# Optimization experiments

Hardware: AMD Instinct MI355X
Metric: run time of the kernel (lower is better)

## Reference

```python
import jax, jax.numpy as jnp
import numpy as np

NPERSEG = 512
STEP = 256
NSEG = 9            # frames for L=2048 with boundary='zeros', padded=True
NFREQ = 257
NUM_FILTER = 2
PI = 3.1415926      # same constant as source

_win = 0.5 * (1.0 - jnp.cos(2.0 * jnp.pi * jnp.arange(NPERSEG, dtype=jnp.float32) / NPERSEG))  # periodic hann (scipy get_window('hann'))
_win_sum = 256.0    # sum of periodic hann, exact


def _stft(x):
    # x: (B, D, L) real -> scipy.signal.stft(..., nperseg=512, noverlap=256) => (B, D, 257, 9)
    xp = jnp.pad(x, ((0, 0), (0, 0), (STEP, STEP)))  # boundary='zeros'
    idx = jnp.arange(NSEG)[:, None] * STEP + jnp.arange(NPERSEG)[None, :]
    frames = xp[..., idx] * _win                     # (B,D,9,512)
    Z = jnp.fft.rfft(frames, axis=-1) / _win_sum     # scaling='spectrum'
    return jnp.swapaxes(Z, -1, -2)                   # (B,D,257,9)


def _istft(Z):
    # Z: (B,D,257,9) complex -> (B,D,2048) real (scipy.signal.istft inverse)
    xs = jnp.fft.irfft(jnp.swapaxes(Z, -1, -2) * _win_sum, n=NPERSEG, axis=-1) * _win  # (B,D,9,512)
    total = NPERSEG + (NSEG - 1) * STEP  # 2560
    idx = (jnp.arange(NSEG)[:, None] * STEP + jnp.arange(NPERSEG)[None, :]).reshape(-1)
    B, D = Z.shape[0], Z.shape[1]
    x = jnp.zeros((B, D, total), xs.dtype).at[..., idx].add(xs.reshape(B, D, -1))
    norm = jnp.zeros((total,), jnp.float32).at[idx].add(jnp.tile(_win ** 2, NSEG))
    x = x / jnp.where(norm > 1e-10, norm, 1.0)
    return x[..., STEP:total - STEP]  # trim boundary padding -> length 2048


def _cplx(p):
    return p[..., 0] + 1j * p[..., 1]  # torch.view_as_complex


def _filter(x, length, bank):
    # x: (B,S,D) complex; bank: (K,S,D,2). power = x*x/length (complex square, as in source)
    power = x * x / length
    k = jnp.arange(NUM_FILTER, dtype=jnp.float32)
    coef = jnp.cos((2.0 * (k + 1.0) - 1.0) * PI / 2.0 * NUM_FILTER)  # matches source precedence
    return jnp.sum(power[None] * _cplx(bank)[:, None] * coef[:, None, None, None], axis=0)


def _ln(x, g, b):
    m = jnp.mean(x, -1, keepdims=True)
    v = jnp.mean((x - m) ** 2, -1, keepdims=True)
    return (x - m) * jax.lax.rsqrt(v + 1e-5) * g + b


def _addnorm(x, g1, b1, w1, bb1, w2, bb2, g2, b2):
    x = _ln(x, g1, b1)
    h = jax.nn.gelu(x @ w1.T + bb1, approximate=False)  # torch GELU (exact)
    return _ln(h @ w2.T + bb2 + x, g2, b2)


def setup_inputs() -> dict:
    key = jax.random.key(0)
    ks = jax.random.split(key, 12)
    B, D = 8, 768
    d = {}
    d['ecg'] = jax.random.normal(ks[0], (B, 2048, D), jnp.float32)
    d['image'] = jax.random.normal(ks[1], (B, 196, D), jnp.float32)
    d['ecg_filter_bank'] = jax.random.normal(ks[2], (2, 2313, D, 2), jnp.float32)
    d['cxr_filter_bank'] = jax.random.normal(ks[3], (2, 99, D, 2), jnp.float32)
    d['gate_sel'] = jax.random.normal(ks[4], (99, D, 2), jnp.float32)
    d['gate_w'] = jax.random.normal(ks[5], (D, D), jnp.float32) * 0.02
    d['gate_b'] = jnp.zeros((D,), jnp.float32)
    for i, p in enumerate(['e', 'c']):
        d[p + '_ln1_g'] = jnp.ones((D,), jnp.float32)
        d[p + '_ln1_b'] = jnp.zeros((D,), jnp.float32)
        d[p + '_w1'] = jax.random.normal(ks[6 + 2 * i], (D, D), jnp.float32) * 0.02
        d[p + '_b1'] = jnp.zeros((D,), jnp.float32)
        d[p + '_w2'] = jax.random.normal(ks[7 + 2 * i], (D, D), jnp.float32) * 0.02
        d[p + '_b2'] = jnp.zeros((D,), jnp.float32)
        d[p + '_ln2_g'] = jnp.ones((D,), jnp.float32)
        d[p + '_ln2_b'] = jnp.zeros((D,), jnp.float32)
    return d


def reference(ecg, image, ecg_filter_bank, cxr_filter_bank, gate_sel, gate_w, gate_b,
              e_ln1_g, e_ln1_b, e_w1, e_b1, e_w2, e_b2, e_ln2_g, e_ln2_b,
              c_ln1_g, c_ln1_b, c_w1, c_b1, c_w2, c_b2, c_ln2_g, c_ln2_b):
    B, S, D = ecg.shape
    N = image.shape[1]
    # STFT path (source detaches to CPU -> stop_gradient)
    Z = _stft(jnp.swapaxes(jax.lax.stop_gradient(ecg), 1, 2))       # (B,D,257,9)
    _ecg = jnp.transpose(Z, (0, 2, 3, 1)).reshape(B, NFREQ * NSEG, D)
    _img = jnp.fft.rfft(image, axis=1, norm='ortho')                # (B,99,D)
    _ecg = _filter(_ecg, NFREQ * NSEG, ecg_filter_bank)
    _img = _filter(_img, N // 2 + 1, cxr_filter_bank)
    # Cxr2EcgGate: complex selection, avgpool over spatial (real part), 1x1 conv
    gate = jnp.mean((_img * _cplx(gate_sel)).real, axis=1) @ gate_w.T + gate_b  # (B,D)
    ecg_g = _ecg * gate[:, None, :]
    # NOTE: source overwrites gated image with irfft of filtered _image (ecg_gate output unused)
    img_t = jnp.fft.irfft(_img, n=N, axis=1, norm='ortho')          # (B,N,D)
    Zg = jnp.transpose(ecg_g.reshape(B, NFREQ, NSEG, D), (0, 3, 1, 2))
    ecg_t = jnp.swapaxes(_istft(jax.lax.stop_gradient(Zg)), 1, 2)   # (B,2048,D); source detaches before istft
    text = _addnorm(ecg_t + ecg, e_ln1_g, e_ln1_b, e_w1, e_b1, e_w2, e_b2, e_ln2_g, e_ln2_b)
    img = _addnorm(img_t + image, c_ln1_g, c_ln1_b, c_w1, c_b1, c_w2, c_b2, c_ln2_g, c_ln2_b)
    return (text, img)
```

## Files before the change

kernel.cpp:

```cpp
#include <hip/hip_runtime.h>
#include <math.h>

namespace {

constexpr int B_ = 8;
constexpr int S_ = 2048;
constexpr int D_ = 768;
constexpr int N_ = 196;
constexpr int NF_ = 99;
constexpr int NFREQ_ = 257;
constexpr int NSEG_ = 9;
constexpr int NBINS_ = NFREQ_ * NSEG_;
constexpr int NW_ = D_ * D_;
constexpr float TWOPI_ = 6.28318530717958647692f;

using bf16x8 = __attribute__((ext_vector_type(8))) short;
using f32x4  = __attribute__((ext_vector_type(4))) float;

__device__ __forceinline__ int rev9(int x) { return (int)(__brev((unsigned)x) >> 23); }
__device__ __forceinline__ int padz(int i) { return i + (i >> 4); }

__device__ __forceinline__ unsigned short f2bf(float x) {
  unsigned u = __float_as_uint(x);
  u = (u + 0x7FFFu + ((u >> 16) & 1u)) >> 16;
  return (unsigned short)u;
}
__device__ __forceinline__ float bf2f(unsigned short h) {
  return __uint_as_float(((unsigned)h) << 16);
}

__device__ __forceinline__ float gelu_f(float v) {
  const float x = fabsf(v) * 0.70710678118654752440f;
  const float t = 1.0f / fmaf(0.3275911f, x, 1.0f);
  float p = fmaf(fmaf(fmaf(fmaf(1.061405429f, t, -1.453152027f), t, 1.421413741f),
                      t, -0.284496736f), t, 0.254829592f);
  const float e = __expf(-x * x);
  const float er = 1.0f - p * t * e;
  return 0.5f * v * (1.0f + ((v < 0.f) ? -er : er));
}

__device__ __forceinline__ void gload16(const void* g, void* l) {
  __builtin_amdgcn_global_load_lds((const __attribute__((address_space(1))) void*)g,
                                   (__attribute__((address_space(3))) void*)l, 16, 0, 0);
}

__device__ __forceinline__ float2 cmulf(float2 a, float2 b) {
  return make_float2(a.x * b.x - a.y * b.y, a.x * b.y + a.y * b.x);
}
__device__ __forceinline__ float2 cadd(float2 a, float2 b) {
  return make_float2(a.x + b.x, a.y + b.y);
}
__device__ __forceinline__ float2 csub(float2 a, float2 b) {
  return make_float2(a.x - b.x, a.y - b.y);
}

__global__ __launch_bounds__(256) void k_transpose_g(const float* __restrict__ src,
                                                     float* __restrict__ dst,
                                                     int R, int C) {
  __shared__ float tile[32][33];
  const int b = blockIdx.z;
  const int c0 = blockIdx.x * 32;
  const int r0 = blockIdx.y * 32;
  const int tx = threadIdx.x & 31, ty = threadIdx.x >> 5;
  for (int i = ty; i < 32; i += 8)
    tile[i][tx] = src[((size_t)b * R + r0 + i) * C + c0 + tx];
  __syncthreads();
  for (int i = ty; i < 32; i += 8)
    dst[((size_t)b * C + c0 + i) * R + r0 + tx] = tile[tx][i];
}

constexpr int PREP_W = (NW_ + 255) / 256;
constexpr int PREP_WALL = 4 * PREP_W;
constexpr int PREP_FC = (NBINS_ * D_ + 255) / 256;
__global__ __launch_bounds__(256) void k_prep(
    const float* __restrict__ w0, const float* __restrict__ w1,
    const float* __restrict__ w2, const float* __restrict__ w3,
    unsigned short* __restrict__ wbf, const float2* __restrict__ e2,
    float2* __restrict__ FcT, float2* __restrict__ twg) {
  const int bid = blockIdx.x;
  if (bid < PREP_WALL) {
    const int m = bid / PREP_W;
    const int i = (bid - m * PREP_W) * 256 + threadIdx.x;
    if (i >= NW_) return;
    const float* src = (m == 0) ? w0 : (m == 1) ? w1 : (m == 2) ? w2 : w3;
    wbf[(size_t)m * NW_ + i] = f2bf(src[i]);
  } else if (bid < PREP_WALL + PREP_FC) {
    const int o = (bid - PREP_WALL) * 256 + threadIdx.x;
    if (o >= NBINS_ * D_) return;
    const int d = o / NBINS_;
    const int r = o - d * NBINS_;
    const int f = r / NFREQ_;
    const int k = r - f * NFREQ_;
    const int s = k * 9 + f;
    const float2 a = e2[(size_t)s * D_ + d];
    const float2 b = e2[(size_t)(NBINS_ + s) * D_ + d];
    FcT[o] = make_float2(-(a.x + b.x), -(a.y + b.y));
  } else {
    const int i = (bid - PREP_WALL - PREP_FC) * 256 + threadIdx.x;
    if (i >= 511) return;
    const int v = i + 1;
    const int h = 1 << (31 - __clz(v));
    const int j = v - h;
    float sn, cs;
    sincosf((float)j * ((TWOPI_ * 0.5f) / (float)h), &sn, &cs);
    twg[i] = make_float2(cs, sn);
  }
}

__global__ __launch_bounds__(256) void k_img_dft_f(
    const float* __restrict__ image, const float2* __restrict__ bank2,
    const float2* __restrict__ gsel2, float2* __restrict__ imgF,
    float* __restrict__ part) {
  const int fg = blockIdx.x;
  const int f0 = fg * 9;
  const int d = blockIdx.y * 256 + threadIdx.x;
  const int b = blockIdx.z;
  __shared__ float2 tws[9 * N_];
  for (int idx = threadIdx.x; idx < 9 * N_; idx += 256) {
    const int fi = idx / N_;
    const int t = idx - fi * N_;
    const int r = ((f0 + fi) * t) % N_;
    float sn, cs;
    sincosf(TWOPI_ * (float)r / (float)N_, &sn, &cs);
    tws[idx] = make_float2(cs, sn);
  }
  __syncthreads();
  float re[9] = {}, im[9] = {};
  const float* ip = image + (size_t)b * N_ * D_ + d;
  for (int t = 0; t < N_; ++t) {
    const float v = ip[(size_t)t * D_];
#pragma unroll
    for (int fi = 0; fi < 9; ++fi) {
      const float2 w = tws[fi * N_ + t];
      re[fi] = fmaf(v, w.x, re[fi]);
      im[fi] = fmaf(-v, w.y, im[fi]);
    }
  }
  const float sc = 1.0f / (196.0f * 99.0f);
  float gp = 0.f;
#pragma unroll
  for (int fi = 0; fi < 9; ++fi) {
    const int f = f0 + fi;
    const float pr = (re[fi] * re[fi] - im[fi] * im[fi]) * sc;
    const float pi2 = (2.f * re[fi] * im[fi]) * sc;
    const size_t fd = (size_t)f * D_ + d;
    const float2 c0 = bank2[fd];
    const float2 c1 = bank2[(size_t)NF_ * D_ + fd];
    const float fcr = -(c0.x + c1.x), fci = -(c0.y + c1.y);
    const float zr = pr * fcr - pi2 * fci;
    const float zi = pr * fci + pi2 * fcr;
    imgF[(size_t)(b * NF_ + f) * D_ + d] = make_float2(zr, zi);
    const float2 gw = gsel2[fd];
    gp += zr * gw.x - zi * gw.y;
  }
  part[((size_t)b * 11 + fg) * D_ + d] = gp;
}

__global__ __launch_bounds__(256) void k_gate_mm2(const float* __restrict__ part,
                                                  const float* __restrict__ W,
                                                  const float* __restrict__ bias,
                                                  float* __restrict__ gate) {
  __shared__ float row[8][D_];
  __shared__ float red[16][16][8];
  const int tid = threadIdx.x;
  const int d0 = blockIdx.x * 16;
  for (int i = tid; i < 8 * D_; i += 256) {
    const int b = i / D_, e = i - b * D_;
    float s = 0.f;
    for (int p = 0; p < 11; ++p) s += part[((size_t)b * 11 + p) * D_ + e];
    row[b][e] = s * (1.0f / 99.0f);
  }
  __syncthreads();
  const int dl = tid >> 4;
  const int ec = tid & 15;
  const float* w = W + (size_t)(d0 + dl) * D_ + ec * 48;
  float acc[8] = {};
  for (int e = 0; e < 48; e += 4) {
    const float4 wv = *reinterpret_cast<const float4*>(w + e);
    const int eg = ec * 48 + e;
#pragma unroll
    for (int b = 0; b < 8; ++b) {
      acc[b] = fmaf(row[b][eg], wv.x, acc[b]);
      acc[b] = fmaf(row[b][eg + 1], wv.y, acc[b]);
      acc[b] = fmaf(row[b][eg + 2], wv.z, acc[b]);
      acc[b] = fmaf(row[b][eg + 3], wv.w, acc[b]);
    }
  }
#pragma unroll
  for (int b = 0; b < 8; ++b) red[dl][ec][b] = acc[b];
  __syncthreads();
  if (tid < 128) {
    const int dl2 = tid >> 3, b = tid & 7;
    float s = bias[d0 + dl2];
    for (int c = 0; c < 16; ++c) s += red[dl2][c][b];
    gate[b * D_ + d0 + dl2] = s;
  }
}

__global__ __launch_bounds__(256) void k_img_idft(
    const float2* __restrict__ imgF, const float* __restrict__ image,
    float* __restrict__ xi) {
  const int t0 = blockIdx.x * 14;
  const int d = blockIdx.y * 256 + threadIdx.x;
  const int b = blockIdx.z;
  __shared__ float2 tws[14 * NF_];
  for (int idx = threadIdx.x; idx < 14 * NF_; idx += 256) {
    const int ti = idx / NF_;
    const int f = idx - ti * NF_;
    const int r = ((t0 + ti) * f) % N_;
    float sn, cs;
    sincosf(TWOPI_ * (float)r / (float)N_, &sn, &cs);
    tws[idx] = make_float2(cs, sn);
  }
  __syncthreads();
  const float2* zp = imgF + (size_t)b * NF_ * D_ + d;
  const float2 z0 = zp[0];
  const float2 zny = zp[(size_t)(NF_ - 1) * D_];
  float acc[14];
#pragma unroll
  for (int ti = 0; ti < 14; ++ti)
    acc[ti] = z0.x + (((t0 + ti) & 1) ? -zny.x : zny.x);
  for (int f = 1; f < NF_ - 1; ++f) {
    const float2 z = zp[(size_t)f * D_];
#pragma unroll
    for (int ti = 0; ti < 14; ++ti) {
      const float2 w = tws[ti * NF_ + f];
      acc[ti] += 2.f * (z.x * w.x - z.y * w.y);
    }
  }
#pragma unroll
  for (int ti = 0; ti < 14; ++ti) {
    const size_t idx = (size_t)(b * N_ + t0 + ti) * D_ + d;
    xi[idx] = acc[ti] * (1.0f / 14.0f) + image[idx];
  }
}

__global__ __launch_bounds__(256) void k_layernorm_f2b(const float* __restrict__ x,
                                                       const float* __restrict__ g,
                                                       const float* __restrict__ b,
                                                       unsigned short* __restrict__ out) {
  const int row = blockIdx.x;
  const int tid = threadIdx.x;
  const float* xr = x + (size_t)row * D_;
  const float v0 = xr[tid], v1 = xr[tid + 256], v2 = xr[tid + 512];
  float s = v0 + v1 + v2;
  float q = v0 * v0 + v1 * v1 + v2 * v2;
  __shared__ float red[8];
  for (int off = 32; off > 0; off >>= 1) {
    s += __shfl_down(s, off);
    q += __shfl_down(q, off);
  }
  if ((tid & 63) == 0) { red[tid >> 6] = s; red[4 + (tid >> 6)] = q; }
  __syncthreads();
  s = red[0] + red[1] + red[2] + red[3];
  q = red[4] + red[5] + red[6] + red[7];
  const float mean = s * (1.0f / 768.0f);
  const float var = q * (1.0f / 768.0f) - mean * mean;
  const float inv = rsqrtf(var + 1e-5f);
  unsigned short* orow = out + (size_t)row * D_;
  orow[tid]       = f2bf((v0 - mean) * inv * g[tid]       + b[tid]);
  orow[tid + 256] = f2bf((v1 - mean) * inv * g[tid + 256] + b[tid + 256]);
  orow[tid + 512] = f2bf((v2 - mean) * inv * g[tid + 512] + b[tid + 512]);
}

template <int H, int DIR, bool TRIV>
__device__ __forceinline__ void pass8(float2* z, int l,
                                      float2 wa, float2 wb, float2 wc) {
  asm volatile("s_waitcnt lgkmcnt(0)" ::: "memory");
  const float sg = (DIR < 0) ? -1.f : 1.f;
  const int base = (H == 1) ? (l << 3)
                 : (H == 8) ? (((l >> 3) << 6) | (l & 7))
                            : l;
  const float2 x0 = z[padz(base)],         x1 = z[padz(base + H)];
  const float2 x2 = z[padz(base + 2 * H)], x3 = z[padz(base + 3 * H)];
  const float2 x4 = z[padz(base + 4 * H)], x5 = z[padz(base + 5 * H)];
  const float2 x6 = z[padz(base + 6 * H)], x7 = z[padz(base + 7 * H)];
  const float2 WA = make_float2(wa.x, sg * wa.y);
  const float2 WB = make_float2(wb.x, sg * wb.y);
  const float2 WC = make_float2(wc.x, sg * wc.y);
  const float2 WBp = make_float2(-sg * WB.y, sg * WB.x);
  float2 t, u;
  t = TRIV ? x1 : cmulf(x1, WA); const float2 A0 = cadd(x0, t), A1 = csub(x0, t);
  t = TRIV ? x3 : cmulf(x3, WA); const float2 A2 = cadd(x2, t), A3 = csub(x2, t);
  t = TRIV ? x5 : cmulf(x5, WA); const float2 A4 = cadd(x4, t), A5 = csub(x4, t);
  t = TRIV ? x7 : cmulf(x7, WA); const float2 A6 = cadd(x6, t), A7 = csub(x6, t);
  t = TRIV ? A2 : cmulf(A2, WB);
  u = TRIV ? make_float2(-sg * A3.y, sg * A3.x) : cmulf(A3, WBp);
  const float2 B0 = cadd(A0, t), B2 = csub(A0, t);
  const float2 B1 = cadd(A1, u), B3 = csub(A1, u);
  t = TRIV ? A6 : cmulf(A6, WB);
  u = TRIV ? make_float2(-sg * A7.y, sg * A7.x) : cmulf(A7, WBp);
  const float2 B4 = cadd(A4, t), B6 = csub(A4, t);
  const float2 B5 = cadd(A5, u), B7 = csub(A5, u);
  const float r_ = 0.70710678118654752440f;
  const float2 F1 = TRIV ? make_float2(r_, sg * r_)
                         : cmulf(WC, make_float2(r_, sg * r_));
  const float2 F2 = TRIV ? make_float2(0.f, sg)
                         : make_float2(-sg * WC.y, sg * WC.x);
  const float2 F3 = TRIV ? make_float2(-r_, sg * r_)
                         : cmulf(WC, make_float2(-r_, sg * r_));
  t = TRIV ? B4 : cmulf(B4, WC);
  z[padz(base)]         = cadd(B0, t);
  z[padz(base + 4 * H)] = csub(B0, t);
  t = cmulf(B5, F1);
  z[padz(base + H)]     = cadd(B1, t);
  z[padz(base + 5 * H)] = csub(B1, t);
  t = cmulf(B6, F2);
  z[padz(base + 2 * H)] = cadd(B2, t);
  z[padz(base + 6 * H)] = csub(B2, t);
  t = cmulf(B7, F3);
  z[padz(base + 3 * H)] = cadd(B3, t);
  z[padz(base + 7 * H)] = csub(B3, t);
}

template <int FA, int FB>
__device__ __forceinline__ void filt_pack(const float2* z, int k, float g,
                                          float2 cA, float2 cB,
                                          float2& Ck, float2& Cm) {
  const int q = (512 - k) & 511;
  const float2 Zk = z[padz(k)], Zq = z[padz(q)];
  const float sc = 0.5f / 256.f;
  const float ar = (Zk.x + Zq.x) * sc, ai = (Zk.y - Zq.y) * sc;
  float yar, yai, ybr = 0.f, ybi = 0.f;
  {
    const float pr = (ar * ar - ai * ai) * (1.f / 2313.f);
    const float pi = (2.f * ar * ai) * (1.f / 2313.f);
    yar = (pr * cA.x - pi * cA.y) * g;
    yai = (pr * cA.y + pi * cA.x) * g;
  }
  if (FB >= 0) {
    const float br = (Zk.y + Zq.y) * sc, bi = (Zq.x - Zk.x) * sc;
    const float pr = (br * br - bi * bi) * (1.f / 2313.f);
    const float pi = (2.f * br * bi) * (1.f / 2313.f);
    ybr = (pr * cB.x - pi * cB.y) * g;
    ybi = (pr * cB.y + pi * cB.x) * g;
  }
  if (k == 0 || k == 256) {
    Ck = make_float2(yar, ybr);
    Cm = Ck;
  } else {
    Ck = make_float2(yar - ybi, yai + ybr);
    Cm = make_float2(yar + ybi, ybr - yai);
  }
}

template <int FA0, int FB0, int FA1, int FB1, bool DUAL>
__device__ __forceinline__ void ecg_super(int tid, float g, const float2* __restrict__ fc,
                                          const float (&s)[8], const float2 (&ptw)[6],
                                          float2 t8, float2* zA, float2* zB, float* accr) {
  const float c0 = t8.x;
  const float wlo = 0.5f - 0.5f * c0;
  const float whi = 0.5f + 0.5f * c0;
  const float2 cA0 = fc[FA0 * 257 + tid];
  float2 cB0 = make_float2(0.f, 0.f), cA1 = cB0, cB1 = cB0;
  if (FB0 >= 0) cB0 = fc[FB0 * 257 + tid];
  if (DUAL) { cA1 = fc[FA1 * 257 + tid]; cB1 = fc[FB1 * 257 + tid]; }
  float2 nA0 = make_float2(0.f, 0.f), nB0 = nA0, nA1 = nA0, nB1 = nA0;
  if (tid == 0) {
    nA0 = fc[FA0 * 257 + 256];
    if (FB0 >= 0) nB0 = fc[FB0 * 257 + 256];
    if (DUAL) { nA1 = fc[FA1 * 257 + 256]; nB1 = fc[FB1 * 257 + 256]; }
  }
  __syncthreads();
  {
    constexpr int iAlo = (FA0 > 0) ? FA0 - 1 : 0;
    constexpr int iAhi = (FA0 < 8) ? FA0 : 0;
    constexpr int iBlo = (FB0 > 0) ? FB0 - 1 : 0;
    constexpr int iBhi = (FB0 >= 0 && FB0 < 8) ? FB0 : 0;
    const int rlo = padz(rev9(tid)), rhi = padz(rev9(tid + 256));
    const float aLo = (FA0 == 0) ? 0.f : s[iAlo] * wlo;
    const float aHi = (FA0 == 8) ? 0.f : s[iAhi] * whi;
    const float bLo = (FB0 <= 0) ? 0.f : s[iBlo] * wlo;
    const float bHi = (FB0 < 0 || FB0 == 8) ? 0.f : s[iBhi] * whi;
    zA[rlo] = make_float2(aLo, bLo);
    zA[rhi] = make_float2(aHi, bHi);
    if (DUAL) {
      constexpr int jAlo = (FA1 > 0) ? FA1 - 1 : 0;
      constexpr int jAhi = (FA1 < 8) ? FA1 : 0;
      constexpr int jBlo = (FB1 > 0) ? FB1 - 1 : 0;
      constexpr int jBhi = (FB1 < 8) ? FB1 : 0;
      const float eLo = (FA1 == 0) ? 0.f : s[jAlo] * wlo;
      const float eHi = (FA1 == 8) ? 0.f : s[jAhi] * whi;
      const float fLo = (FB1 == 0) ? 0.f : s[jBlo] * wlo;
      const float fHi = (FB1 == 8) ? 0.f : s[jBhi] * whi;
      zB[rlo] = make_float2(eLo, fLo);
      zB[rhi] = make_float2(eHi, fHi);
    }
  }
  __syncthreads();
  if (tid < 64 || (DUAL && tid >= 128 && tid < 192)) {
    float2* zz = (tid < 64) ? zA : zB;
    const int l = tid & 63;
    pass8<1, -1, true>(zz, l, ptw[0], ptw[1], ptw[2]);
    pass8<8, -1, false>(zz, l, ptw[0], ptw[1], ptw[2]);
    pass8<64, -1, false>(zz, l, ptw[3], ptw[4], ptw[5]);
  }
  __syncthreads();
  float2 CAk, CAm, CBk, CBm;
  filt_pack<FA0, FB0>(zA, tid, g, cA0, cB0, CAk, CAm);
  float2 CAn, CBn, dum;
  if (tid == 0) filt_pack<FA0, FB0>(zA, 256, g, nA0, nB0, CAn, dum);
  if (DUAL) {
    filt_pack<FA1, FB1>(zB, tid, g, cA1, cB1, CBk, CBm);
    if (tid == 0) filt_pack<FA1, FB1>(zB, 256, g, nA1, nB1, CBn, dum);
  }
  __syncthreads();
  {
    const int rk = padz(rev9(tid));
    zA[rk] = CAk;
    if (DUAL) zB[rk] = CBk;
    if (tid == 0) {
      zA[padz(1)] = CAn;
      if (DUAL) zB[padz(1)] = CBn;
    } else {
      const int rm = padz(rev9(512 - tid));
      zA[rm] = CAm;
      if (DUAL) zB[rm] = CBm;
    }
  }
  __syncthreads();
  if (tid < 64 || (DUAL && tid >= 128 && tid < 192)) {
    float2* zz = (tid < 64) ? zA : zB;
    const int l = tid & 63;
    pass8<1, 1, true>(zz, l, ptw[0], ptw[1], ptw[2]);
    pass8<8, 1, false>(zz, l, ptw[0], ptw[1], ptw[2]);
    pass8<64, 1, false>(zz, l, ptw[3], ptw[4], ptw[5]);
  }
  __syncthreads();
  {
    const float2 vLo = zA[padz(tid)], vHi = zA[padz(tid + 256)];
    accr[FA0] += 0.5f * wlo * vLo.x;
    accr[FA0 + 1] += 0.5f * whi * vHi.x;
    if (FB0 >= 0) {
      accr[FB0] += 0.5f * wlo * vLo.y;
      accr[FB0 + 1] += 0.5f * whi * vHi.y;
    }
    if (DUAL) {
      const float2 uLo = zB[padz(tid)], uHi = zB[padz(tid + 256)];
      accr[FA1] += 0.5f * wlo * uLo.x;
      accr[FA1 + 1] += 0.5f * whi * uHi.x;
      accr[FB1] += 0.5f * wlo * uLo.y;
      accr[FB1 + 1] += 0.5f * whi * uHi.y;
    }
  }
}

__global__ __launch_bounds__(256) void k_ecg_fft(
    const float* __restrict__ ecgT, const float2* __restrict__ FcT,
    const float* __restrict__ gate, const float2* __restrict__ twg,
    unsigned short* __restrict__ xtT) {
  const int bd = blockIdx.x;
  const int d = bd % D_;
  const int tid = threadIdx.x;

  __shared__ float2 zA[544], zB[544];

  float s[8];
  const float* src = ecgT + (size_t)bd * S_;
#pragma unroll
  for (int k = 0; k < 8; ++k) s[k] = src[k * 256 + tid];

  const int l6 = tid & 63;
  float2 ptw[6];
  ptw[0] = twg[7 + (l6 & 7)];
  ptw[1] = twg[15 + (l6 & 7)];
  ptw[2] = twg[31 + (l6 & 7)];
  ptw[3] = twg[63 + l6];
  ptw[4] = twg[127 + l6];
  ptw[5] = twg[255 + l6];
  const float2 t8 = twg[255 + tid];

  const float g = gate[bd];
  const float2* fc = FcT + (size_t)d * NBINS_;
  float accr[10];
#pragma unroll
  for (int i = 0; i < 10; ++i) accr[i] = 0.f;

  ecg_super<0, 8, 1, 2, true>(tid, g, fc, s, ptw, t8, zA, zB, accr);
  ecg_super<3, 4, 5, 6, true>(tid, g, fc, s, ptw, t8, zA, zB, accr);
  ecg_super<7, -1, 0, 0, false>(tid, g, fc, s, ptw, t8, zA, zB, accr);

  const float c0 = t8.x;
  const float rinv = 1.0f / (0.5f + 0.5f * c0 * c0);
  unsigned short* dst = xtT + (size_t)bd * S_;
#pragma unroll
  for (int i2 = 0; i2 < 8; ++i2)
    dst[i2 * 256 + tid] = f2bf(accr[i2 + 1] * rinv + s[i2]);
}

__global__ __launch_bounds__(256) void k_colstats_bf(const unsigned short* __restrict__ xtT,
                                                     float2* __restrict__ stats) {
  const int b = blockIdx.y;
  const int t0 = blockIdx.x * 128;
  const int tx = threadIdx.x & 63;
  const int ty = threadIdx.x >> 6;
  float s0 = 0.f, q0 = 0.f, s1 = 0.f, q1 = 0.f;
  const unsigned int* base = (const unsigned int*)(xtT + (size_t)b * D_ * S_);
  for (int dd = ty; dd < D_; dd += 4) {
    const unsigned int u = base[(size_t)dd * (S_ / 2) + (t0 >> 1) + tx];
    const float v0 = bf2f((unsigned short)(u & 0xffffu));
    const float v1 = bf2f((unsigned short)(u >> 16));
    s0 += v0; q0 = fmaf(v0, v0, q0);
    s1 += v1; q1 = fmaf(v1, v1, q1);
  }
  __shared__ float sh[4][64][4];
  sh[ty][tx][0] = s0; sh[ty][tx][1] = q0; sh[ty][tx][2] = s1; sh[ty][tx][3] = q1;
  __syncthreads();
  if (ty == 0) {
    s0 = sh[0][tx][0] + sh[1][tx][0] + sh[2][tx][0] + sh[3][tx][0];
    q0 = sh[0][tx][1] + sh[1][tx][1] + sh[2][tx][1] + sh[3][tx][1];
    s1 = sh[0][tx][2] + sh[1][tx][2] + sh[2][tx][2] + sh[3][tx][2];
    q1 = sh[0][tx][3] + sh[1][tx][3] + sh[2][tx][3] + sh[3][tx][3];
    stats[(size_t)b * S_ + t0 + 2 * tx]     = make_float2(s0, q0);
    stats[(size_t)b * S_ + t0 + 2 * tx + 1] = make_float2(s1, q1);
  }
}

__global__ __launch_bounds__(256) void k_transpose_ln(
    const unsigned short* __restrict__ xtT, const float2* __restrict__ stats,
    const float* __restrict__ g, const float* __restrict__ bia,
    unsigned short* __restrict__ xhat) {
  __shared__ float tile[32][33];
  const int b = blockIdx.z;
  const int t0 = blockIdx.x * 32;
  const int d0 = blockIdx.y * 32;
  const int tx = threadIdx.x & 31, ty = threadIdx.x >> 5;
  for (int i = ty; i < 32; i += 8)
    tile[i][tx] = bf2f(xtT[((size_t)b * D_ + d0 + i) * S_ + t0 + tx]);
  __syncthreads();
  const float gv = g[d0 + tx], bv = bia[d0 + tx];
  for (int i = ty; i < 32; i += 8) {
    const float2 st = stats[(size_t)b * S_ + t0 + i];
    const float mean = st.x * (1.0f / 768.0f);
    const float var = st.y * (1.0f / 768.0f) - mean * mean;
    const float inv = rsqrtf(var + 1e-5f);
    xhat[((size_t)b * S_ + t0 + i) * D_ + d0 + tx] =
        f2bf((tile[tx][i] - mean) * inv * gv + bv);
  }
}

__global__ __launch_bounds__(256) void k_layernorm_bf(const unsigned short* __restrict__ x,
                                                      const float* __restrict__ g,
                                                      const float* __restrict__ b,
                                                      float* __restrict__ out) {
  const int row = blockIdx.x;
  const int tid = threadIdx.x;
  const unsigned short* xr = x + (size_t)row * D_;
  const float v0 = bf2f(xr[tid]), v1 = bf2f(xr[tid + 256]), v2 = bf2f(xr[tid + 512]);
  float s = v0 + v1 + v2;
  float q = v0 * v0 + v1 * v1 + v2 * v2;
  __shared__ float red[8];
  for (int off = 32; off > 0; off >>= 1) {
    s += __shfl_down(s, off);
    q += __shfl_down(q, off);
  }
  if ((tid & 63) == 0) { red[tid >> 6] = s; red[4 + (tid >> 6)] = q; }
  __syncthreads();
  s = red[0] + red[1] + red[2] + red[3];
  q = red[4] + red[5] + red[6] + red[7];
  const float mean = s * (1.0f / 768.0f);
  const float var = q * (1.0f / 768.0f) - mean * mean;
  const float inv = rsqrtf(var + 1e-5f);
  float* orow = out + (size_t)row * D_;
  orow[tid]       = (v0 - mean) * inv * g[tid]       + b[tid];
  orow[tid + 256] = (v1 - mean) * inv * g[tid + 256] + b[tid + 256];
  orow[tid + 512] = (v2 - mean) * inv * g[tid + 512] + b[tid + 512];
}

template <int MODE, bool SWZ>
__global__ __launch_bounds__(256) void k_gemm_mfma(
    const unsigned short* __restrict__ Abf, const unsigned short* __restrict__ Wbf,
    const float* __restrict__ bias, const unsigned short* __restrict__ resid,
    unsigned short* __restrict__ outb, int M) {
  __shared__ unsigned short Asm[2][128 * 64];
  __shared__ unsigned short Bsm[2][128 * 64];
  const int tid = threadIdx.x;
  const int lane = tid & 63, wid = tid >> 6;
  const int wr = wid >> 1, wc = wid & 1;
  int bx = blockIdx.x, by = blockIdx.y;
  if (SWZ) {
    const int nwg = gridDim.x * gridDim.y;
    const int bid = by * gridDim.x + bx;
    const int nbid = (bid % 8) * (nwg >> 3) + (bid >> 3);
    bx = nbid % gridDim.x;
    by = nbid / gridDim.x;
  }
  const int n0 = bx * 128, m0 = by * 128;

  auto STAGE = [&](int buf, int kt) {
    const int k0 = kt * 64;
#pragma unroll
    for (int i = 0; i < 4; ++i) {
      const int c = tid + 256 * i;
      const int row = c >> 3, sl = c & 7;
      const int gsl = sl ^ (row & 7);
      gload16(Abf + (size_t)(m0 + row) * 768 + k0 + gsl * 8, &Asm[buf][c * 8]);
      gload16(Wbf + (size_t)(n0 + row) * 768 + k0 + gsl * 8, &Bsm[buf][c * 8]);
    }
  };

  f32x4 acc[4][4] = {};
  STAGE(0, 0);
  for (int kt = 0; kt < 12; ++kt) {
    const int cur = kt & 1;
    if (kt < 11) {
      STAGE(cur ^ 1, kt + 1);
      asm volatile("s_waitcnt vmcnt(8)" ::: "memory");
    } else {
      asm volatile("s_waitcnt vmcnt(0)" ::: "memory");
    }
    __builtin_amdgcn_sched_barrier(0);
    __builtin_amdgcn_s_barrier();
#pragma unroll
    for (int ks = 0; ks < 2; ++ks) {
      bf16x8 af[4], bfv[4];
#pragma unroll
      for (int mi = 0; mi < 4; ++mi) {
        const int row = wr * 64 + mi * 16 + (lane & 15);
        const int sl = (ks * 4 + (lane >> 4)) ^ (row & 7);
        af[mi] = *(const bf16x8*)((const char*)Asm[cur] + row * 128 + sl * 16);
      }
#pragma unroll
      for (int ni = 0; ni < 4; ++ni) {
        const int row = wc * 64 + ni * 16 + (lane & 15);
        const int sl = (ks * 4 + (lane >> 4)) ^ (row & 7);
        bfv[ni] = *(const bf16x8*)((const char*)Bsm[cur] + row * 128 + sl * 16);
      }
#pragma unroll
      for (int mi = 0; mi < 4; ++mi)
#pragma unroll
        for (int ni = 0; ni < 4; ++ni)
          acc[mi][ni] = __builtin_amdgcn_mfma_f32_16x16x32_bf16(af[mi], bfv[ni],
                                                                acc[mi][ni], 0, 0, 0);
    }
    __builtin_amdgcn_sched_barrier(0);
    __builtin_amdgcn_s_barrier();
  }
#pragma unroll
  for (int mi = 0; mi < 4; ++mi) {
#pragma unroll
    for (int ni = 0; ni < 4; ++ni) {
      const int col = n0 + wc * 64 + ni * 16 + (lane & 15);
#pragma unroll
      for (int e = 0; e < 4; ++e) {
        const int row = m0 + wr * 64 + mi * 16 + (lane >> 4) * 4 + e;
        if (row >= M) continue;
        float v = acc[mi][ni][e] + bias[col];
        if (MODE == 0) {
          v = gelu_f(v);
        } else {
          v += bf2f(resid[(size_t)row * 768 + col]);
        }
        outb[(size_t)row * 768 + col] = f2bf(v);
      }
    }
  }
}

}

extern "C" void kernel_launch(void* const* d_in, const int* in_sizes, int n_in,
                              void* d_out, int out_size, void* d_ws, size_t ws_size,
                              hipStream_t stream) {
  (void)in_sizes; (void)n_in; (void)out_size; (void)ws_size;
  const float* ecg     = (const float*)d_in[0];
  const float* image   = (const float*)d_in[1];
  const float* ebank   = (const float*)d_in[2];
  const float* cbank   = (const float*)d_in[3];
  const float* gsel    = (const float*)d_in[4];
  const float* gw      = (const float*)d_in[5];
  const float* gb      = (const float*)d_in[6];
  const float* e_ln1_g = (const float*)d_in[7];
  const float* e_ln1_b = (const float*)d_in[8];
  const float* e_w1    = (const float*)d_in[9];
  const float* e_b1    = (const float*)d_in[10];
  const float* e_w2    = (const float*)d_in[11];
  const float* e_b2    = (const float*)d_in[12];
  const float* e_ln2_g = (const float*)d_in[13];
  const float* e_ln2_b = (const float*)d_in[14];
  const float* c_ln1_g = (const float*)d_in[15];
  const float* c_ln1_b = (const float*)d_in[16];
  const float* c_w1    = (const float*)d_in[17];
  const float* c_b1    = (const float*)d_in[18];
  const float* c_w2    = (const float*)d_in[19];
  const float* c_b2    = (const float*)d_in[20];
  const float* c_ln2_g = (const float*)d_in[21];
  const float* c_ln2_b = (const float*)d_in[22];

  float* out = (float*)d_out;
  float* ws = (float*)d_ws;

  constexpr size_t TXT = (size_t)8 * 2048 * 768;
  constexpr size_t IMG = (size_t)8 * 196 * 768;

  float* A  = ws;
  float* Bb = A + TXT;
  unsigned short* wbf = (unsigned short*)(Bb + TXT);
  unsigned short* ew1b = wbf;
  unsigned short* ew2b = wbf + NW_;
  unsigned short* cw1b = wbf + 2 * NW_;
  unsigned short* cw2b = wbf + 3 * NW_;
  float* gatev = (float*)(wbf + 4 * (size_t)NW_);
  float2* stats = (float2*)(gatev + 8 * 768);
  float* gpart = (float*)(stats + 8 * 2048);
  float2* twg = (float2*)(gpart + 8 * 11 * 768);

  float2* FcT = (float2*)out;

  float* xi = A;
  unsigned short* xh_i = (unsigned short*)(A + IMG);
  unsigned short* h_i  = xh_i + IMG;
  unsigned short* y_ib = h_i + IMG;

  unsigned short* xhat = (unsigned short*)A;
  unsigned short* y_tb = (unsigned short*)A + TXT;
  unsigned short* xtT  = (unsigned short*)Bb;
  unsigned short* h_t  = (unsigned short*)Bb;

  k_prep<<<PREP_WALL + PREP_FC + 2, 256, 0, stream>>>(
      e_w1, e_w2, c_w1, c_w2, wbf, (const float2*)ebank, FcT, twg);

  k_img_dft_f<<<dim3(11, 3, 8), 256, 0, stream>>>(image, (const float2*)cbank,
                                                  (const float2*)gsel,
                                                  (float2*)(A + 2 * IMG), gpart);
  k_gate_mm2<<<48, 256, 0, stream>>>(gpart, gw, gb, gatev);
  k_img_idft<<<dim3(14, 3, 8), 256, 0, stream>>>((const float2*)(A + 2 * IMG), image, xi);
  k_layernorm_f2b<<<1568, 256, 0, stream>>>(xi, c_ln1_g, c_ln1_b, xh_i);
  k_gemm_mfma<0, false><<<dim3(6, 13), 256, 0, stream>>>(xh_i, cw1b, c_b1, nullptr, h_i, 1568);
  k_gemm_mfma<1, false><<<dim3(6, 13), 256, 0, stream>>>(h_i, cw2b, c_b2, xh_i, y_ib, 1568);
  k_layernorm_bf<<<1568, 256, 0, stream>>>(y_ib, c_ln2_g, c_ln2_b, out + TXT);

  k_transpose_g<<<dim3(24, 64, 8), 256, 0, stream>>>(ecg, A, 2048, 768);
  k_ecg_fft<<<8 * 768, 256, 0, stream>>>(A, FcT, gatev, twg, xtT);
  k_colstats_bf<<<dim3(16, 8), 256, 0, stream>>>(xtT, stats);
  k_transpose_ln<<<dim3(64, 24, 8), 256, 0, stream>>>(xtT, stats, e_ln1_g, e_ln1_b, xhat);

  k_gemm_mfma<0, true><<<dim3(6, 128), 256, 0, stream>>>(xhat, ew1b, e_b1, nullptr, h_t, 16384);
  k_gemm_mfma<1, true><<<dim3(6, 128), 256, 0, stream>>>(h_t, ew2b, e_b2, xhat, y_tb, 16384);
  k_layernorm_bf<<<16384, 256, 0, stream>>>(y_tb, e_ln2_g, e_ln2_b, out);
}
```

Baseline: 474.6 us.

## Batch four FFT buffers per pass and merge image/ECG GEMM and layernorm launches

The ECG STFT kernel now processes four frame-pair buffers per super-step using all four wavefronts, so two super-steps replace three and fewer block barriers are needed. The image-branch GEMMs and final layernorm are merged into the ECG-branch launches through dual-problem kernels that pick operands by block index. This removes small under-filled launches, and the GEMM gets an XCD swizzle that handles block counts not divisible by 8. To avoid overlap, the image buffers are moved into the upper half of the second workspace. The cost is more shared memory per FFT block, which may lower occupancy.

```diff
diff --git a/kernel.cpp b/kernel.cpp
--- a/kernel.cpp
+++ b/kernel.cpp
@@ -314,6 +314,21 @@
 }
 
 template <int FA, int FB>
+__device__ __forceinline__ void scatter_buf(float2* z, const float (&s)[8],
+                                            float wlo, float whi, int rlo, int rhi) {
+  constexpr int iAlo = (FA > 0) ? FA - 1 : 0;
+  constexpr int iAhi = (FA < 8) ? FA : 0;
+  constexpr int iBlo = (FB > 0) ? FB - 1 : 0;
+  constexpr int iBhi = (FB >= 0 && FB < 8) ? FB : 0;
+  const float aLo = (FA == 0) ? 0.f : s[iAlo] * wlo;
+  const float aHi = (FA == 8) ? 0.f : s[iAhi] * whi;
+  const float bLo = (FB <= 0) ? 0.f : s[iBlo] * wlo;
+  const float bHi = (FB < 0 || FB == 8) ? 0.f : s[iBhi] * whi;
+  z[rlo] = make_float2(aLo, bLo);
+  z[rhi] = make_float2(aHi, bHi);
+}
+
+template <int FA, int FB>
 __device__ __forceinline__ void filt_pack(const float2* z, int k, float g,
                                           float2 cA, float2 cB,
                                           float2& Ck, float2& Cm) {
@@ -344,84 +359,84 @@
   }
 }
 
-template <int FA0, int FB0, int FA1, int FB1, bool DUAL>
-__device__ __forceinline__ void ecg_super(int tid, float g, const float2* __restrict__ fc,
-                                          const float (&s)[8], const float2 (&ptw)[6],
-                                          float2 t8, float2* zA, float2* zB, float* accr) {
+template <int FA0, int FB0, int FA1, int FB1, int FA2, int FB2, int FA3, int FB3,
+          int NBUF>
+__device__ __forceinline__ void ecg_super4(int tid, float g,
+                                           const float2* __restrict__ fc,
+                                           const float (&s)[8], const float2 (&ptw)[6],
+                                           float2 t8, float2* zA, float2* zB,
+                                           float2* zC, float2* zD, float* accr) {
   const float c0 = t8.x;
   const float wlo = 0.5f - 0.5f * c0;
   const float whi = 0.5f + 0.5f * c0;
-  const float2 cA0 = fc[FA0 * 257 + tid];
+  float2 cA0 = fc[FA0 * 257 + tid];
   float2 cB0 = make_float2(0.f, 0.f), cA1 = cB0, cB1 = cB0;
+  float2 cA2 = cB0, cB2 = cB0, cA3 = cB0, cB3 = cB0;
   if (FB0 >= 0) cB0 = fc[FB0 * 257 + tid];
-  if (DUAL) { cA1 = fc[FA1 * 257 + tid]; cB1 = fc[FB1 * 257 + tid]; }
-  float2 nA0 = make_float2(0.f, 0.f), nB0 = nA0, nA1 = nA0, nB1 = nA0;
-  if (tid == 0) {
-    nA0 = fc[FA0 * 257 + 256];
-    if (FB0 >= 0) nB0 = fc[FB0 * 257 + 256];
-    if (DUAL) { nA1 = fc[FA1 * 257 + 256]; nB1 = fc[FB1 * 257 + 256]; }
-  }
-  __syncthreads();
-  {
-    constexpr int iAlo = (FA0 > 0) ? FA0 - 1 : 0;
-    constexpr int iAhi = (FA0 < 8) ? FA0 : 0;
-    constexpr int iBlo = (FB0 > 0) ? FB0 - 1 : 0;
-    constexpr int iBhi = (FB0 >= 0 && FB0 < 8) ? FB0 : 0;
-    const int rlo = padz(rev9(tid)), rhi = padz(rev9(tid + 256));
-    const float aLo = (FA0 == 0) ? 0.f : s[iAlo] * wlo;
-    const float aHi = (FA0 == 8) ? 0.f : s[iAhi] * whi;
-    const float bLo = (FB0 <= 0) ? 0.f : s[iBlo] * wlo;
-    const float bHi = (FB0 < 0 || FB0 == 8) ? 0.f : s[iBhi] * whi;
-    zA[rlo] = make_float2(aLo, bLo);
-    zA[rhi] = make_float2(aHi, bHi);
-    if (DUAL) {
-      constexpr int jAlo = (FA1 > 0) ? FA1 - 1 : 0;
-      constexpr int jAhi = (FA1 < 8) ? FA1 : 0;
-      constexpr int jBlo = (FB1 > 0) ? FB1 - 1 : 0;
-      constexpr int jBhi = (FB1 < 8) ? FB1 : 0;
-      const float eLo = (FA1 == 0) ? 0.f : s[jAlo] * wlo;
-      const float eHi = (FA1 == 8) ? 0.f : s[jAhi] * whi;
-      const float fLo = (FB1 == 0) ? 0.f : s[jBlo] * wlo;
-      const float fHi = (FB1 == 8) ? 0.f : s[jBhi] * whi;
-      zB[rlo] = make_float2(eLo, fLo);
-      zB[rhi] = make_float2(eHi, fHi);
-    }
-  }
-  __syncthreads();
-  if (tid < 64 || (DUAL && tid >= 128 && tid < 192)) {
-    float2* zz = (tid < 64) ? zA : zB;
-    const int l = tid & 63;
+  if (NBUF > 1) { cA1 = fc[FA1 * 257 + tid]; cB1 = fc[FB1 * 257 + tid]; }
+  if (NBUF > 2) { cA2 = fc[FA2 * 257 + tid]; cB2 = fc[FB2 * 257 + tid]; }
+  if (NBUF > 3) { cA3 = fc[FA3 * 257 + tid]; cB3 = fc[FB3 * 257 + tid]; }
+  __syncthreads();
+  const int rlo = padz(rev9(tid)), rhi = padz(rev9(tid + 256));
+  scatter_buf<FA0, FB0>(zA, s, wlo, whi, rlo, rhi);
+  if (NBUF > 1) scatter_buf<FA1, FB1>(zB, s, wlo, whi, rlo, rhi);
+  if (NBUF > 2) scatter_buf<FA2, FB2>(zC, s, wlo, whi, rlo, rhi);
+  if (NBUF > 3) scatter_buf<FA3, FB3>(zD, s, wlo, whi, rlo, rhi);
+  __syncthreads();
+  const int wid = tid >> 6, l = tid & 63;
+  if (wid < NBUF) {
+    float2* zz = (wid == 0) ? zA : (wid == 1) ? zB : (wid == 2) ? zC : zD;
     pass8<1, -1, true>(zz, l, ptw[0], ptw[1], ptw[2]);
     pass8<8, -1, false>(zz, l, ptw[0], ptw[1], ptw[2]);
     pass8<64, -1, false>(zz, l, ptw[3], ptw[4], ptw[5]);
   }
   __syncthreads();
-  float2 CAk, CAm, CBk, CBm;
-  filt_pack<FA0, FB0>(zA, tid, g, cA0, cB0, CAk, CAm);
-  float2 CAn, CBn, dum;
-  if (tid == 0) filt_pack<FA0, FB0>(zA, 256, g, nA0, nB0, CAn, dum);
-  if (DUAL) {
-    filt_pack<FA1, FB1>(zB, tid, g, cA1, cB1, CBk, CBm);
-    if (tid == 0) filt_pack<FA1, FB1>(zB, 256, g, nA1, nB1, CBn, dum);
+  float2 Ck0, Cm0, Ck1, Cm1, Ck2, Cm2, Ck3, Cm3;
+  float2 Cn0, Cn1, Cn2, Cn3, dum;
+  filt_pack<FA0, FB0>(zA, tid, g, cA0, cB0, Ck0, Cm0);
+  if (NBUF > 1) filt_pack<FA1, FB1>(zB, tid, g, cA1, cB1, Ck1, Cm1);
+  if (NBUF > 2) filt_pack<FA2, FB2>(zC, tid, g, cA2, cB2, Ck2, Cm2);
+  if (NBUF > 3) filt_pack<FA3, FB3>(zD, tid, g, cA3, cB3, Ck3, Cm3);
+  if (tid == 0) {
+    float2 nA, nB = make_float2(0.f, 0.f);
+    nA = fc[FA0 * 257 + 256];
+    if (FB0 >= 0) nB = fc[FB0 * 257 + 256];
+    filt_pack<FA0, FB0>(zA, 256, g, nA, nB, Cn0, dum);
+    if (NBUF > 1) {
+      nA = fc[FA1 * 257 + 256]; nB = fc[FB1 * 257 + 256];
+      filt_pack<FA1, FB1>(zB, 256, g, nA, nB, Cn1, dum);
+    }
+    if (NBUF > 2) {
+      nA = fc[FA2 * 257 + 256]; nB = fc[FB2 * 257 + 256];
+      filt_pack<FA2, FB2>(zC, 256, g, nA, nB, Cn2, dum);
+    }
+    if (NBUF > 3) {
+      nA = fc[FA3 * 257 + 256]; nB = fc[FB3 * 257 + 256];
+      filt_pack<FA3, FB3>(zD, 256, g, nA, nB, Cn3, dum);
+    }
   }
   __syncthreads();
   {
-    const int rk = padz(rev9(tid));
-    zA[rk] = CAk;
-    if (DUAL) zB[rk] = CBk;
+    zA[rlo] = Ck0;
+    if (NBUF > 1) zB[rlo] = Ck1;
+    if (NBUF > 2) zC[rlo] = Ck2;
+    if (NBUF > 3) zD[rlo] = Ck3;
     if (tid == 0) {
-      zA[padz(1)] = CAn;
-      if (DUAL) zB[padz(1)] = CBn;
+      zA[padz(1)] = Cn0;
+      if (NBUF > 1) zB[padz(1)] = Cn1;
+      if (NBUF > 2) zC[padz(1)] = Cn2;
+      if (NBUF > 3) zD[padz(1)] = Cn3;
     } else {
       const int rm = padz(rev9(512 - tid));
-      zA[rm] = CAm;
-      if (DUAL) zB[rm] = CBm;
-    }
-  }
-  __syncthreads();
-  if (tid < 64 || (DUAL && tid >= 128 && tid < 192)) {
-    float2* zz = (tid < 64) ? zA : zB;
-    const int l = tid & 63;
+      zA[rm] = Cm0;
+      if (NBUF > 1) zB[rm] = Cm1;
+      if (NBUF > 2) zC[rm] = Cm2;
+      if (NBUF > 3) zD[rm] = Cm3;
+    }
+  }
+  __syncthreads();
+  if (wid < NBUF) {
+    float2* zz = (wid == 0) ? zA : (wid == 1) ? zB : (wid == 2) ? zC : zD;
     pass8<1, 1, true>(zz, l, ptw[0], ptw[1], ptw[2]);
     pass8<8, 1, false>(zz, l, ptw[0], ptw[1], ptw[2]);
     pass8<64, 1, false>(zz, l, ptw[3], ptw[4], ptw[5]);
@@ -435,12 +450,26 @@
       accr[FB0] += 0.5f * wlo * vLo.y;
       accr[FB0 + 1] += 0.5f * whi * vHi.y;
     }
-    if (DUAL) {
+    if (NBUF > 1) {
       const float2 uLo = zB[padz(tid)], uHi = zB[padz(tid + 256)];
       accr[FA1] += 0.5f * wlo * uLo.x;
       accr[FA1 + 1] += 0.5f * whi * uHi.x;
       accr[FB1] += 0.5f * wlo * uLo.y;
       accr[FB1 + 1] += 0.5f * whi * uHi.y;
+    }
+    if (NBUF > 2) {
+      const float2 uLo = zC[padz(tid)], uHi = zC[padz(tid + 256)];
+      accr[FA2] += 0.5f * wlo * uLo.x;
+      accr[FA2 + 1] += 0.5f * whi * uHi.x;
+      accr[FB2] += 0.5f * wlo * uLo.y;
+      accr[FB2 + 1] += 0.5f * whi * uHi.y;
+    }
+    if (NBUF > 3) {
+      const float2 uLo = zD[padz(tid)], uHi = zD[padz(tid + 256)];
+      accr[FA3] += 0.5f * wlo * uLo.x;
+      accr[FA3 + 1] += 0.5f * whi * uHi.x;
+      accr[FB3] += 0.5f * wlo * uLo.y;
+      accr[FB3 + 1] += 0.5f * whi * uHi.y;
     }
   }
 }
@@ -453,7 +482,7 @@
   const int d = bd % D_;
   const int tid = threadIdx.x;
 
-  __shared__ float2 zA[544], zB[544];
+  __shared__ float2 zA[544], zB[544], zC[544], zD[544];
 
   float s[8];
   const float* src = ecgT + (size_t)bd * S_;
@@ -476,9 +505,8 @@
 #pragma unroll
   for (int i = 0; i < 10; ++i) accr[i] = 0.f;
 
-  ecg_super<0, 8, 1, 2, true>(tid, g, fc, s, ptw, t8, zA, zB, accr);
-  ecg_super<3, 4, 5, 6, true>(tid, g, fc, s, ptw, t8, zA, zB, accr);
-  ecg_super<7, -1, 0, 0, false>(tid, g, fc, s, ptw, t8, zA, zB, accr);
+  ecg_super4<0, 8, 1, 2, 3, 4, 5, 6, 4>(tid, g, fc, s, ptw, t8, zA, zB, zC, zD, accr);
+  ecg_super4<7, -1, 0, 0, 0, 0, 0, 0, 1>(tid, g, fc, s, ptw, t8, zA, zB, zC, zD, accr);
 
   const float c0 = t8.x;
   const float rinv = 1.0f / (0.5f + 0.5f * c0 * c0);
@@ -539,11 +567,15 @@
   }
 }
 
-__global__ __launch_bounds__(256) void k_layernorm_bf(const unsigned short* __restrict__ x,
-                                                      const float* __restrict__ g,
-                                                      const float* __restrict__ b,
-                                                      float* __restrict__ out) {
-  const int row = blockIdx.x;
+__global__ __launch_bounds__(256) void k_layernorm_dual(
+    const unsigned short* __restrict__ x1, const float* __restrict__ g1,
+    const float* __restrict__ b1, float* __restrict__ o1, int n1,
+    const unsigned short* __restrict__ x2, const float* __restrict__ g2,
+    const float* __restrict__ b2, float* __restrict__ o2) {
+  int row = blockIdx.x;
+  const unsigned short* x; const float *g, *b; float* o;
+  if (row < n1) { x = x1; g = g1; b = b1; o = o1; }
+  else { row -= n1; x = x2; g = g2; b = b2; o = o2; }
   const int tid = threadIdx.x;
   const unsigned short* xr = x + (size_t)row * D_;
   const float v0 = bf2f(xr[tid]), v1 = bf2f(xr[tid + 256]), v2 = bf2f(xr[tid + 512]);
@@ -561,30 +593,40 @@
   const float mean = s * (1.0f / 768.0f);
   const float var = q * (1.0f / 768.0f) - mean * mean;
   const float inv = rsqrtf(var + 1e-5f);
-  float* orow = out + (size_t)row * D_;
+  float* orow = o + (size_t)row * D_;
   orow[tid]       = (v0 - mean) * inv * g[tid]       + b[tid];
   orow[tid + 256] = (v1 - mean) * inv * g[tid + 256] + b[tid + 256];
   orow[tid + 512] = (v2 - mean) * inv * g[tid + 512] + b[tid + 512];
 }
 
-template <int MODE, bool SWZ>
-__global__ __launch_bounds__(256) void k_gemm_mfma(
-    const unsigned short* __restrict__ Abf, const unsigned short* __restrict__ Wbf,
-    const float* __restrict__ bias, const unsigned short* __restrict__ resid,
-    unsigned short* __restrict__ outb, int M) {
+template <int MODE>
+__global__ __launch_bounds__(256) void k_gemm_dual(
+    const unsigned short* __restrict__ A1, const unsigned short* __restrict__ W1,
+    const float* __restrict__ b1, const unsigned short* __restrict__ r1,
+    unsigned short* __restrict__ o1, int M1, int nby1,
+    const unsigned short* __restrict__ A2, const unsigned short* __restrict__ W2,
+    const float* __restrict__ b2, const unsigned short* __restrict__ r2,
+    unsigned short* __restrict__ o2, int M2) {
   __shared__ unsigned short Asm[2][128 * 64];
   __shared__ unsigned short Bsm[2][128 * 64];
   const int tid = threadIdx.x;
   const int lane = tid & 63, wid = tid >> 6;
   const int wr = wid >> 1, wc = wid & 1;
-  int bx = blockIdx.x, by = blockIdx.y;
-  if (SWZ) {
+  int bx, by;
+  {
     const int nwg = gridDim.x * gridDim.y;
-    const int bid = by * gridDim.x + bx;
-    const int nbid = (bid % 8) * (nwg >> 3) + (bid >> 3);
+    const int bid = blockIdx.y * gridDim.x + blockIdx.x;
+    const int xcd = bid & 7, lin = bid >> 3;
+    const int qq = nwg >> 3, rr = nwg & 7;
+    const int nbid = (xcd < rr) ? xcd * (qq + 1) + lin
+                                : rr * (qq + 1) + (xcd - rr) * qq + lin;
     bx = nbid % gridDim.x;
     by = nbid / gridDim.x;
   }
+  const unsigned short* Abf; const unsigned short* Wbf; const float* bias;
+  const unsigned short* resid; unsigned short* outb; int M;
+  if (by < nby1) { Abf = A1; Wbf = W1; bias = b1; resid = r1; outb = o1; M = M1; }
+  else { by -= nby1; Abf = A2; Wbf = W2; bias = b2; resid = r2; outb = o2; M = M2; }
   const int n0 = bx * 128, m0 = by * 128;
 
   auto STAGE = [&](int buf, int kt) {
@@ -707,35 +749,38 @@
 
   float2* FcT = (float2*)out;
 
-  float* xi = A;
-  unsigned short* xh_i = (unsigned short*)(A + IMG);
+  unsigned short* xhat = (unsigned short*)A;
+  unsigned short* y_tb = (unsigned short*)A + TXT;
+  unsigned short* xtT = (unsigned short*)Bb;
+  unsigned short* h_t = (unsigned short*)Bb;
+  float* Bb2 = Bb + TXT / 2;
+  float2* imgF = (float2*)Bb2;
+  float* xi = Bb2 + 1216512;
+  unsigned short* xh_i = (unsigned short*)(xi + IMG);
   unsigned short* h_i  = xh_i + IMG;
   unsigned short* y_ib = h_i + IMG;
 
-  unsigned short* xhat = (unsigned short*)A;
-  unsigned short* y_tb = (unsigned short*)A + TXT;
-  unsigned short* xtT  = (unsigned short*)Bb;
-  unsigned short* h_t  = (unsigned short*)Bb;
-
   k_prep<<<PREP_WALL + PREP_FC + 2, 256, 0, stream>>>(
       e_w1, e_w2, c_w1, c_w2, wbf, (const float2*)ebank, FcT, twg);
 
   k_img_dft_f<<<dim3(11, 3, 8), 256, 0, stream>>>(image, (const float2*)cbank,
-                                                  (const float2*)gsel,
-                                                  (float2*)(A + 2 * IMG), gpart);
+                                                  (const float2*)gsel, imgF, gpart);
   k_gate_mm2<<<48, 256, 0, stream>>>(gpart, gw, gb, gatev);
-  k_img_idft<<<dim3(14, 3, 8), 256, 0, stream>>>((const float2*)(A + 2 * IMG), image, xi);
+  k_img_idft<<<dim3(14, 3, 8), 256, 0, stream>>>(imgF, image, xi);
   k_layernorm_f2b<<<1568, 256, 0, stream>>>(xi, c_ln1_g, c_ln1_b, xh_i);
-  k_gemm_mfma<0, false><<<dim3(6, 13), 256, 0, stream>>>(xh_i, cw1b, c_b1, nullptr, h_i, 1568);
-  k_gemm_mfma<1, false><<<dim3(6, 13), 256, 0, stream>>>(h_i, cw2b, c_b2, xh_i, y_ib, 1568);
-  k_layernorm_bf<<<1568, 256, 0, stream>>>(y_ib, c_ln2_g, c_ln2_b, out + TXT);
 
   k_transpose_g<<<dim3(24, 64, 8), 256, 0, stream>>>(ecg, A, 2048, 768);
   k_ecg_fft<<<8 * 768, 256, 0, stream>>>(A, FcT, gatev, twg, xtT);
   k_colstats_bf<<<dim3(16, 8), 256, 0, stream>>>(xtT, stats);
   k_transpose_ln<<<dim3(64, 24, 8), 256, 0, stream>>>(xtT, stats, e_ln1_g, e_ln1_b, xhat);
 
-  k_gemm_mfma<0, true><<<dim3(6, 128), 256, 0, stream>>>(xhat, ew1b, e_b1, nullptr, h_t, 16384);
-  k_gemm_mfma<1, true><<<dim3(6, 128), 256, 0, stream>>>(h_t, ew2b, e_b2, xhat, y_tb, 16384);
-  k_layernorm_bf<<<16384, 256, 0, stream>>>(y_tb, e_ln2_g, e_ln2_b, out);
-}
+  k_gemm_dual<0><<<dim3(6, 141), 256, 0, stream>>>(
+      xhat, ew1b, e_b1, nullptr, h_t, 16384, 128,
+      xh_i, cw1b, c_b1, nullptr, h_i, 1568);
+  k_gemm_dual<1><<<dim3(6, 141), 256, 0, stream>>>(
+      h_t, ew2b, e_b2, xhat, y_tb, 16384, 128,
+      h_i, cw2b, c_b2, xh_i, y_ib, 1568);
+  k_layernorm_dual<<<16384 + 1568, 256, 0, stream>>>(
+      y_tb, e_ln2_g, e_ln2_b, out, 16384,
+      y_ib, c_ln2_g, c_ln2_b, out + TXT);
+}
```

New measurement: 413.5 us. 12.9% less time.
